# Optimization experiments

Hardware: AMD Instinct MI355X
Metric: run time of the kernel (lower is better)

Reference implementation:

```python
import jax, jax.numpy as jnp
import numpy as np

B, N, C = 64, 1024, 128


def setup_inputs() -> dict:
    key = jax.random.key(0)
    k1, k2, k3, k4, k5, k6 = jax.random.split(key, 6)
    adj_vals = jax.random.uniform(k1, (B, N, N), dtype=jnp.float32)
    mask = jax.random.uniform(k2, (B, N, N)) < 0.1
    adjacent = jnp.where(mask, adj_vals, 0.0)
    annotations = jax.random.normal(k3, (B, N, C), dtype=jnp.float32)
    # GraphConvolution bias, shape (1,1,C)
    gc_bias = jax.random.normal(k4, (1, 1, C), dtype=jnp.float32) * 0.05
    # Keras GRU params (reset_after=True default): kernel (C,3C), recurrent (C,3C), bias (2,3C)
    kernel = jax.random.normal(k5, (C, 3 * C), dtype=jnp.float32) / np.sqrt(C)
    recurrent_kernel = jax.random.normal(k6, (C, 3 * C), dtype=jnp.float32) / np.sqrt(C)
    gru_bias = jnp.zeros((2, 3 * C), dtype=jnp.float32)
    return {"adjacent": adjacent, "annotations": annotations, "gc_bias": gc_bias,
            "kernel": kernel, "recurrent_kernel": recurrent_kernel, "gru_bias": gru_bias}


def reference(adjacent, annotations, gc_bias, kernel, recurrent_kernel, gru_bias):
    # GraphConvolution: per-graph adj @ annotations, batched, + bias
    v = jnp.einsum('bij,bjc->bic', adjacent, annotations) + gc_bias  # [B,N,C]
    b, n, c = v.shape
    x = v.reshape(-1, c)            # visible states, one GRU step each
    h = annotations.reshape(-1, c)  # initial hidden states
    # single-step Keras GRU (reset_after=True)
    mx = x @ kernel + gru_bias[0]
    mh = h @ recurrent_kernel + gru_bias[1]
    xz, xr, xh = jnp.split(mx, 3, axis=-1)
    hz, hr, hh_in = jnp.split(mh, 3, axis=-1)
    z = jax.nn.sigmoid(xz + hz)
    r = jax.nn.sigmoid(xr + hr)
    hh = jnp.tanh(xh + r * hh_in)
    out = z * h + (1.0 - z) * hh
    return out.reshape(b, n, c)
```

## Files before the change

### kernel.cpp

```cpp
#include <hip/hip_runtime.h>

typedef unsigned short ushort_t;
typedef __attribute__((ext_vector_type(8))) short bf16x8;
typedef __attribute__((ext_vector_type(8))) unsigned short u16x8;
typedef __attribute__((ext_vector_type(4))) float f32x4;

#define B_ 64
#define N_ 1024
#define C_ 128

static __device__ __forceinline__ unsigned short f2bf(float f) {
  union { float f; unsigned int i; } v; v.f = f;
  unsigned int i = v.i;
  return (unsigned short)((i + 0x7FFFu + ((i >> 16) & 1u)) >> 16);
}
static __device__ __forceinline__ void split1(float x, ushort_t& h, ushort_t& l) {
  union { float f; unsigned int i; } u; u.f = x;
  h = (ushort_t)(u.i >> 16);
  union { unsigned int i; float f; } t; t.i = u.i & 0xFFFF0000u;
  union { float f; unsigned int i; } w; w.f = x - t.f;
  l = (ushort_t)(w.i >> 16);
}
static __device__ __forceinline__ bf16x8 as_bf(u16x8 v) {
  union { u16x8 u; bf16x8 b; } x; x.u = v; return x.b;
}
static __device__ __forceinline__ void gload_lds16(const void* g, void* l) {
  __builtin_amdgcn_global_load_lds((const __attribute__((address_space(1))) void*)g,
                                   (__attribute__((address_space(3))) void*)l,
                                   16, 0, 0);
}

#define PIPE_BAR(N) asm volatile("s_waitcnt vmcnt(" #N ")\n\ts_barrier" ::: "memory")
#define POST_BAR()  asm volatile("s_waitcnt lgkmcnt(0)\n\ts_barrier" ::: "memory")

__global__ __launch_bounds__(256) void tsplit(const float* __restrict__ src,
                                              ushort_t* __restrict__ dh,
                                              ushort_t* __restrict__ dl,
                                              int rows, int cols, long sb, long db) {
  __shared__ float tile[64][65];
  const int t = threadIdx.x;
  src += (long)blockIdx.z * sb;
  dh  += (long)blockIdx.z * db;
  dl  += (long)blockIdx.z * db;
  const int r0 = blockIdx.y * 64, c0 = blockIdx.x * 64;
#pragma unroll
  for (int p = 0; p < 4; ++p) {
    int row = p * 16 + (t >> 4), c4 = (t & 15) * 4;
    f32x4 v = *(const f32x4*)(src + (long)(r0 + row) * cols + c0 + c4);
#pragma unroll
    for (int j = 0; j < 4; ++j) tile[row][c4 + j] = v[j];
  }
  __syncthreads();
  const int oc = t >> 2;
#pragma unroll
  for (int p = 0; p < 2; ++p) {
    int ck = (t & 3) + p * 4;
    u16x8 vh, vl;
#pragma unroll
    for (int j = 0; j < 8; ++j) {
      ushort_t hj, lj;
      split1(tile[ck * 8 + j][oc], hj, lj);
      vh[j] = hj; vl[j] = lj;
    }
    long o = (long)(c0 + oc) * rows + r0 + ck * 8;
    *(u16x8*)(dh + o) = vh;
    *(u16x8*)(dl + o) = vl;
  }
}

__global__ __launch_bounds__(256, 2) void gc_gru(const float* __restrict__ adj,
                                                 const ushort_t* __restrict__ annTh,
                                                 const ushort_t* __restrict__ annTl,
                                                 const float* __restrict__ ann,
                                                 const float* __restrict__ gcb,
                                                 const ushort_t* __restrict__ kTh,
                                                 const ushort_t* __restrict__ kTl,
                                                 const ushort_t* __restrict__ rTh,
                                                 const float* __restrict__ gb,
                                                 float* __restrict__ out) {
  __shared__ __align__(16) float vlds[128 * 132];
  float* lds_all = vlds;

  const int tid = threadIdx.x;
  const int w = tid >> 6, lane = tid & 63;
  const int wr = w >> 1, wc = w & 1;
  const int swz = (blockIdx.x & 7) * 64 + (blockIdx.x >> 3);
  const int b = swz >> 3;
  const int m0 = (swz & 7) * 128;

  const float*    adjb = adj   + ((long)b * N_ + m0) * N_;
  const ushort_t* aThb = annTh + (long)b * C_ * N_;
  const ushort_t* aTlb = annTl + (long)b * C_ * N_;

  const int fr = lane & 15;
  const int kg = lane >> 4;

  const int aRow = lane >> 3;
  const int aCs  = (lane & 7) ^ aRow;
  const int bRow = lane >> 2;
  const int bCs  = (lane & 3) ^ ((lane >> 3) & 3);

  f32x4 acc[4][4] = {};

#define STAGE(Q, T)                                                            \
  {                                                                            \
    const int k0_ = (T) * 32;                                                  \
    float*    A_  = lds_all + (Q) * 8192;                                      \
    ushort_t* Bh_ = (ushort_t*)(lds_all + (Q) * 8192 + 4096);                  \
    ushort_t* Bl_ = (ushort_t*)(lds_all + (Q) * 8192 + 6144);                  \
    _Pragma("unroll")                                                          \
    for (int jj = 0; jj < 4; ++jj) {                                           \
      int j_ = w * 4 + jj;                                                     \
      gload_lds16(adjb + (long)(j_ * 8 + aRow) * N_ + k0_ + aCs * 4,           \
                  (void*)(A_ + j_ * 256));                                     \
    }                                                                          \
    _Pragma("unroll")                                                          \
    for (int jj = 0; jj < 2; ++jj) {                                           \
      int j_ = w * 2 + jj;                                                     \
      long so_ = (long)(j_ * 16 + bRow) * N_ + k0_ + bCs * 8;                  \
      gload_lds16(aThb + so_, (void*)(Bh_ + j_ * 512));                        \
      gload_lds16(aTlb + so_, (void*)(Bl_ + j_ * 512));                        \
    }                                                                          \
  }

#define COMPUTE(Q)                                                             \
  {                                                                            \
    const float*    A_  = lds_all + (Q) * 8192;                                \
    const ushort_t* Bh_ = (const ushort_t*)(lds_all + (Q) * 8192 + 4096);      \
    const ushort_t* Bl_ = (const ushort_t*)(lds_all + (Q) * 8192 + 6144);      \
    bf16x8 bh_[4], bl_[4], ah_[4], al_[4];                                     \
    _Pragma("unroll")                                                          \
    for (int ni = 0; ni < 4; ++ni) {                                           \
      int row_ = wc * 64 + ni * 16 + fr;                                       \
      int kb_ = (kg << 4) ^ ((((row_) >> 1) & 3) << 4);                        \
      bh_[ni] = *(const bf16x8*)((const char*)Bh_ + row_ * 64 + kb_);          \
      bl_[ni] = *(const bf16x8*)((const char*)Bl_ + row_ * 64 + kb_);          \
    }                                                                          \
    _Pragma("unroll")                                                          \
    for (int mi = 0; mi < 4; ++mi) {                                           \
      int row_ = wr * 64 + mi * 16 + fr;                                       \
      int b0_ = row_ * 128 + ((kg * 32) ^ ((row_ & 7) << 4));                  \
      f32x4 a0_ = *(const f32x4*)((const char*)A_ + b0_);                      \
      f32x4 a1_ = *(const f32x4*)((const char*)A_ + (b0_ ^ 16));               \
      u16x8 vh_, vl_;                                                          \
      _Pragma("unroll")                                                        \
      for (int j = 0; j < 4; ++j) {                                            \
        ushort_t hj_, lj_;                                                     \
        split1(a0_[j], hj_, lj_); vh_[j] = hj_;     vl_[j] = lj_;              \
        split1(a1_[j], hj_, lj_); vh_[4 + j] = hj_; vl_[4 + j] = lj_;          \
      }                                                                        \
      ah_[mi] = as_bf(vh_); al_[mi] = as_bf(vl_);                              \
    }                                                                          \
    _Pragma("unroll")                                                          \
    for (int mi = 0; mi < 4; ++mi)                                             \
      _Pragma("unroll")                                                        \
      for (int ni = 0; ni < 4; ++ni) {                                         \
        acc[mi][ni] = __builtin_amdgcn_mfma_f32_16x16x32_bf16(ah_[mi], bh_[ni], acc[mi][ni], 0, 0, 0); \
        acc[mi][ni] = __builtin_amdgcn_mfma_f32_16x16x32_bf16(al_[mi], bh_[ni], acc[mi][ni], 0, 0, 0); \
        acc[mi][ni] = __builtin_amdgcn_mfma_f32_16x16x32_bf16(ah_[mi], bl_[ni], acc[mi][ni], 0, 0, 0); \
      }                                                                        \
  }

  STAGE(0, 0)

#pragma unroll 1
  for (int t = 0; t < 31; ++t) {
    const int cur = t & 1;
    STAGE(cur ^ 1, t + 1)
    PIPE_BAR(8);
    COMPUTE(cur)
    POST_BAR();
  }
  PIPE_BAR(0);
  COMPUTE(1)
  __syncthreads();

#undef STAGE
#undef COMPUTE

#pragma unroll
  for (int ni = 0; ni < 4; ++ni) {
    int col = wc * 64 + ni * 16 + fr;
    float bias = gcb[col];
#pragma unroll
    for (int mi = 0; mi < 4; ++mi) {
      int row = wr * 64 + mi * 16 + kg * 4;
#pragma unroll
      for (int r = 0; r < 4; ++r)
        vlds[(row + r) * 132 + col] = acc[mi][ni][r] + bias;
    }
  }
  __syncthreads();

  const long grow = (long)b * N_ + m0 + w * 32;

  bf16x8 xh[2][4], xl[2][4], hh[2][4];
#pragma unroll
  for (int s = 0; s < 2; ++s)
#pragma unroll
    for (int kk = 0; kk < 4; ++kk) {
      int lo = (w * 32 + s * 16 + fr) * 132 + kk * 32 + kg * 8;
      f32x4 x0 = *(const f32x4*)&vlds[lo];
      f32x4 x1 = *(const f32x4*)&vlds[lo + 4];
      u16x8 th, tl;
#pragma unroll
      for (int j = 0; j < 4; ++j) {
        ushort_t hj, lj;
        split1(x0[j], hj, lj); th[j] = hj; tl[j] = lj;
        split1(x1[j], hj, lj); th[4 + j] = hj; tl[4 + j] = lj;
      }
      xh[s][kk] = as_bf(th); xl[s][kk] = as_bf(tl);
      const float* hrow = ann + (grow + s * 16 + fr) * C_ + kk * 32 + kg * 8;
      f32x4 h0 = *(const f32x4*)hrow;
      f32x4 h1 = *(const f32x4*)(hrow + 4);
      u16x8 hv;
#pragma unroll
      for (int j = 0; j < 4; ++j) { hv[j] = f2bf(h0[j]); hv[4 + j] = f2bf(h1[j]); }
      hh[s][kk] = as_bf(hv);
    }

#define GATE(G, AK0, AK1, AR0, AR1)                                                         \
  do {                                                                                      \
    const ushort_t* kh_ = kTh + (long)((G) * C_ + cb) * C_;                                 \
    const ushort_t* kl_ = kTl + (long)((G) * C_ + cb) * C_;                                 \
    const ushort_t* rh_ = rTh + (long)((G) * C_ + cb) * C_;                                 \
    bf16x8 KH[4], KL[4], RH[4];                                                             \
    _Pragma("unroll")                                                                       \
    for (int kk = 0; kk < 4; ++kk) {                                                        \
      int o_ = kk * 32 + kg * 8;                                                            \
      KH[kk] = *(const bf16x8*)(kh_ + o_);                                                  \
      KL[kk] = *(const bf16x8*)(kl_ + o_);                                                  \
      RH[kk] = *(const bf16x8*)(rh_ + o_);                                                  \
    }                                                                                       \
    _Pragma("unroll")                                                                       \
    for (int kk = 0; kk < 4; ++kk) {                                                        \
      AK0 = __builtin_amdgcn_mfma_f32_16x16x32_bf16(xh[0][kk], KH[kk], AK0, 0, 0, 0);       \
      AK1 = __builtin_amdgcn_mfma_f32_16x16x32_bf16(xh[1][kk], KH[kk], AK1, 0, 0, 0);       \
      AK0 = __builtin_amdgcn_mfma_f32_16x16x32_bf16(xl[0][kk], KH[kk], AK0, 0, 0, 0);       \
      AK1 = __builtin_amdgcn_mfma_f32_16x16x32_bf16(xl[1][kk], KH[kk], AK1, 0, 0, 0);       \
      AK0 = __builtin_amdgcn_mfma_f32_16x16x32_bf16(xh[0][kk], KL[kk], AK0, 0, 0, 0);       \
      AK1 = __builtin_amdgcn_mfma_f32_16x16x32_bf16(xh[1][kk], KL[kk], AK1, 0, 0, 0);       \
    }                                                                                       \
    _Pragma("unroll")                                                                       \
    for (int kk = 0; kk < 4; ++kk) {                                                        \
      AR0 = __builtin_amdgcn_mfma_f32_16x16x32_bf16(hh[0][kk], RH[kk], AR0, 0, 0, 0);       \
      AR1 = __builtin_amdgcn_mfma_f32_16x16x32_bf16(hh[1][kk], RH[kk], AR1, 0, 0, 0);       \
    }                                                                                       \
  } while (0)

#pragma unroll 1
  for (int n = 0; n < 8; ++n) {
    const int cb = n * 16 + fr;
    f32x4 az0 = {}, az1 = {}, ar0 = {}, ar1 = {}, ax0 = {}, ax1 = {}, ah0 = {}, ah1 = {};
    GATE(0, az0, az1, az0, az1);
    GATE(1, ar0, ar1, ar0, ar1);
    GATE(2, ax0, ax1, ah0, ah1);

    const float bz  = gb[cb] + gb[384 + cb];
    const float brr = gb[128 + cb] + gb[384 + 128 + cb];
    const float bxh = gb[256 + cb];
    const float bhi = gb[384 + 256 + cb];
#pragma unroll
    for (int s = 0; s < 2; ++s) {
      const f32x4& az_ = s ? az1 : az0;
      const f32x4& ar_ = s ? ar1 : ar0;
      const f32x4& ax_ = s ? ax1 : ax0;
      const f32x4& ah_ = s ? ah1 : ah0;
#pragma unroll
      for (int r = 0; r < 4; ++r) {
        long row = grow + s * 16 + kg * 4 + r;
        float hval = ann[row * C_ + cb];
        float zz = 1.f / (1.f + __expf(-(az_[r] + bz)));
        float rr = 1.f / (1.f + __expf(-(ar_[r] + brr)));
        float hpre = ax_[r] + bxh + rr * (ah_[r] + bhi);
        hpre = fminf(fmaxf(hpre, -15.f), 15.f);
        float e2 = __expf(2.f * hpre);
        float th = (e2 - 1.f) / (e2 + 1.f);
        out[row * C_ + cb] = zz * hval + (1.f - zz) * th;
      }
    }
  }
#undef GATE
}

extern "C" void kernel_launch(void* const* d_in, const int* in_sizes, int n_in,
                              void* d_out, int out_size, void* d_ws, size_t ws_size,
                              hipStream_t stream) {
  const float* adj = (const float*)d_in[0];
  const float* ann = (const float*)d_in[1];
  const float* gcb = (const float*)d_in[2];
  const float* ker = (const float*)d_in[3];
  const float* rk  = (const float*)d_in[4];
  const float* gb  = (const float*)d_in[5];
  float* out = (float*)d_out;

  char* ws = (char*)d_ws;
  ushort_t* annTh = (ushort_t*)(ws);
  ushort_t* annTl = (ushort_t*)(ws + 16777216);
  ushort_t* kTh   = (ushort_t*)(ws + 33554432);
  ushort_t* kTl   = (ushort_t*)(ws + 33652736);
  ushort_t* rTh   = (ushort_t*)(ws + 33751040);
  ushort_t* rTl   = (ushort_t*)(ws + 33849344);

  hipLaunchKernelGGL(tsplit, dim3(2, 16, 64), dim3(256), 0, stream,
                     ann, annTh, annTl, 1024, 128, (long)1024 * 128, (long)128 * 1024);
  hipLaunchKernelGGL(tsplit, dim3(6, 2, 1), dim3(256), 0, stream,
                     ker, kTh, kTl, 128, 384, 0L, 0L);
  hipLaunchKernelGGL(tsplit, dim3(6, 2, 1), dim3(256), 0, stream,
                     rk, rTh, rTl, 128, 384, 0L, 0L);
  hipLaunchKernelGGL(gc_gru, dim3(512), dim3(256), 0, stream,
                     adj, annTh, annTl, ann, gcb, kTh, kTl, rTh, gb, out);
}
```

Before: 163.8 us.

## Restructure GRU epilogue to keep gate weights in registers and pre-split x in LDS

The GRU epilogue is reorganised so each wave owns two 16-column output slices and holds all three gates' weight fragments in registers, looping over the 128 rows. The old layout reloaded the weights from global memory for every gate. The graph-convolution result is now split into bf16 hi/lo once and stored in a swizzled LDS layout, replacing the padded fp32 staging. The transpose kernel also writes a bf16 copy of the annotations so the hidden-state fragments no longer need conversion in the epilogue. Launch bounds drop to one block per SM, which frees registers for the weight fragments but may reduce occupancy for the main matmul loop.

```diff
diff --git a/kernel.cpp b/kernel.cpp
--- a/kernel.cpp
+++ b/kernel.cpp
@@ -3,6 +3,7 @@
 typedef unsigned short ushort_t;
 typedef __attribute__((ext_vector_type(8))) short bf16x8;
 typedef __attribute__((ext_vector_type(8))) unsigned short u16x8;
+typedef __attribute__((ext_vector_type(4))) unsigned short u16x4;
 typedef __attribute__((ext_vector_type(4))) float f32x4;
 
 #define B_ 64
@@ -36,7 +37,9 @@
 __global__ __launch_bounds__(256) void tsplit(const float* __restrict__ src,
                                               ushort_t* __restrict__ dh,
                                               ushort_t* __restrict__ dl,
-                                              int rows, int cols, long sb, long db) {
+                                              ushort_t* __restrict__ db2,
+                                              int rows, int cols, long sb, long db,
+                                              long db2s) {
   __shared__ float tile[64][65];
   const int t = threadIdx.x;
   src += (long)blockIdx.z * sb;
@@ -49,6 +52,12 @@
     f32x4 v = *(const f32x4*)(src + (long)(r0 + row) * cols + c0 + c4);
 #pragma unroll
     for (int j = 0; j < 4; ++j) tile[row][c4 + j] = v[j];
+    if (db2) {
+      u16x4 rb;
+#pragma unroll
+      for (int j = 0; j < 4; ++j) rb[j] = f2bf(v[j]);
+      *(u16x4*)(db2 + (long)blockIdx.z * db2s + (long)(r0 + row) * cols + c0 + c4) = rb;
+    }
   }
   __syncthreads();
   const int oc = t >> 2;
@@ -68,9 +77,10 @@
   }
 }
 
-__global__ __launch_bounds__(256, 2) void gc_gru(const float* __restrict__ adj,
+__global__ __launch_bounds__(256, 1) void gc_gru(const float* __restrict__ adj,
                                                  const ushort_t* __restrict__ annTh,
                                                  const ushort_t* __restrict__ annTl,
+                                                 const ushort_t* __restrict__ annB,
                                                  const float* __restrict__ ann,
                                                  const float* __restrict__ gcb,
                                                  const ushort_t* __restrict__ kTh,
@@ -78,8 +88,7 @@
                                                  const ushort_t* __restrict__ rTh,
                                                  const float* __restrict__ gb,
                                                  float* __restrict__ out) {
-  __shared__ __align__(16) float vlds[128 * 132];
-  float* lds_all = vlds;
+  __shared__ __align__(16) float lds_all[16384];
 
   const int tid = threadIdx.x;
   const int w = tid >> 6, lane = tid & 63;
@@ -94,7 +103,6 @@
 
   const int fr = lane & 15;
   const int kg = lane >> 4;
-
   const int aRow = lane >> 3;
   const int aCs  = (lane & 7) ^ aRow;
   const int bRow = lane >> 2;
@@ -162,7 +170,6 @@
   }
 
   STAGE(0, 0)
-
 #pragma unroll 1
   for (int t = 0; t < 31; ++t) {
     const int cur = t & 1;
@@ -178,101 +185,99 @@
 #undef STAGE
 #undef COMPUTE
 
+  ushort_t* ldsXh = (ushort_t*)lds_all;
+  ushort_t* ldsXl = ldsXh + 16384;
 #pragma unroll
   for (int ni = 0; ni < 4; ++ni) {
     int col = wc * 64 + ni * 16 + fr;
     float bias = gcb[col];
 #pragma unroll
     for (int mi = 0; mi < 4; ++mi) {
-      int row = wr * 64 + mi * 16 + kg * 4;
-#pragma unroll
-      for (int r = 0; r < 4; ++r)
-        vlds[(row + r) * 132 + col] = acc[mi][ni][r] + bias;
+#pragma unroll
+      for (int r = 0; r < 4; ++r) {
+        int row = wr * 64 + mi * 16 + kg * 4 + r;
+        ushort_t hq, lq;
+        split1(acc[mi][ni][r] + bias, hq, lq);
+        int off = row * 256 + ((((col >> 3) ^ (row & 7)) << 4)) + (col & 7) * 2;
+        *(ushort_t*)((char*)ldsXh + off) = hq;
+        *(ushort_t*)((char*)ldsXl + off) = lq;
+      }
     }
   }
   __syncthreads();
 
-  const long grow = (long)b * N_ + m0 + w * 32;
-
-  bf16x8 xh[2][4], xl[2][4], hh[2][4];
-#pragma unroll
-  for (int s = 0; s < 2; ++s)
-#pragma unroll
-    for (int kk = 0; kk < 4; ++kk) {
-      int lo = (w * 32 + s * 16 + fr) * 132 + kk * 32 + kg * 8;
-      f32x4 x0 = *(const f32x4*)&vlds[lo];
-      f32x4 x1 = *(const f32x4*)&vlds[lo + 4];
-      u16x8 th, tl;
-#pragma unroll
-      for (int j = 0; j < 4; ++j) {
-        ushort_t hj, lj;
-        split1(x0[j], hj, lj); th[j] = hj; tl[j] = lj;
-        split1(x1[j], hj, lj); th[4 + j] = hj; tl[4 + j] = lj;
-      }
-      xh[s][kk] = as_bf(th); xl[s][kk] = as_bf(tl);
-      const float* hrow = ann + (grow + s * 16 + fr) * C_ + kk * 32 + kg * 8;
-      f32x4 h0 = *(const f32x4*)hrow;
-      f32x4 h1 = *(const f32x4*)(hrow + 4);
-      u16x8 hv;
-#pragma unroll
-      for (int j = 0; j < 4; ++j) { hv[j] = f2bf(h0[j]); hv[4 + j] = f2bf(h1[j]); }
-      hh[s][kk] = as_bf(hv);
-    }
-
-#define GATE(G, AK0, AK1, AR0, AR1)                                                         \
-  do {                                                                                      \
-    const ushort_t* kh_ = kTh + (long)((G) * C_ + cb) * C_;                                 \
-    const ushort_t* kl_ = kTl + (long)((G) * C_ + cb) * C_;                                 \
-    const ushort_t* rh_ = rTh + (long)((G) * C_ + cb) * C_;                                 \
-    bf16x8 KH[4], KL[4], RH[4];                                                             \
-    _Pragma("unroll")                                                                       \
-    for (int kk = 0; kk < 4; ++kk) {                                                        \
-      int o_ = kk * 32 + kg * 8;                                                            \
-      KH[kk] = *(const bf16x8*)(kh_ + o_);                                                  \
-      KL[kk] = *(const bf16x8*)(kl_ + o_);                                                  \
-      RH[kk] = *(const bf16x8*)(rh_ + o_);                                                  \
-    }                                                                                       \
-    _Pragma("unroll")                                                                       \
-    for (int kk = 0; kk < 4; ++kk) {                                                        \
-      AK0 = __builtin_amdgcn_mfma_f32_16x16x32_bf16(xh[0][kk], KH[kk], AK0, 0, 0, 0);       \
-      AK1 = __builtin_amdgcn_mfma_f32_16x16x32_bf16(xh[1][kk], KH[kk], AK1, 0, 0, 0);       \
-      AK0 = __builtin_amdgcn_mfma_f32_16x16x32_bf16(xl[0][kk], KH[kk], AK0, 0, 0, 0);       \
-      AK1 = __builtin_amdgcn_mfma_f32_16x16x32_bf16(xl[1][kk], KH[kk], AK1, 0, 0, 0);       \
-      AK0 = __builtin_amdgcn_mfma_f32_16x16x32_bf16(xh[0][kk], KL[kk], AK0, 0, 0, 0);       \
-      AK1 = __builtin_amdgcn_mfma_f32_16x16x32_bf16(xh[1][kk], KL[kk], AK1, 0, 0, 0);       \
-    }                                                                                       \
-    _Pragma("unroll")                                                                       \
-    for (int kk = 0; kk < 4; ++kk) {                                                        \
-      AR0 = __builtin_amdgcn_mfma_f32_16x16x32_bf16(hh[0][kk], RH[kk], AR0, 0, 0, 0);       \
-      AR1 = __builtin_amdgcn_mfma_f32_16x16x32_bf16(hh[1][kk], RH[kk], AR1, 0, 0, 0);       \
-    }                                                                                       \
-  } while (0)
+  const long grow = (long)b * N_ + m0;
+  const int frk = fr & 7;
 
 #pragma unroll 1
-  for (int n = 0; n < 8; ++n) {
+  for (int nn = 0; nn < 2; ++nn) {
+    const int n = w * 2 + nn;
+    bf16x8 WKH[3][4], WKL[3][4], WRH[3][4];
+#pragma unroll
+    for (int g = 0; g < 3; ++g) {
+      const long wb = (long)(g * C_ + n * 16 + fr) * C_;
+#pragma unroll
+      for (int kk = 0; kk < 4; ++kk) {
+        int o_ = kk * 32 + kg * 8;
+        WKH[g][kk] = *(const bf16x8*)(kTh + wb + o_);
+        WKL[g][kk] = *(const bf16x8*)(kTl + wb + o_);
+        WRH[g][kk] = *(const bf16x8*)(rTh + wb + o_);
+      }
+    }
+
     const int cb = n * 16 + fr;
-    f32x4 az0 = {}, az1 = {}, ar0 = {}, ar1 = {}, ax0 = {}, ax1 = {}, ah0 = {}, ah1 = {};
-    GATE(0, az0, az1, az0, az1);
-    GATE(1, ar0, ar1, ar0, ar1);
-    GATE(2, ax0, ax1, ah0, ah1);
-
     const float bz  = gb[cb] + gb[384 + cb];
     const float brr = gb[128 + cb] + gb[384 + 128 + cb];
     const float bxh = gb[256 + cb];
     const float bhi = gb[384 + 256 + cb];
-#pragma unroll
-    for (int s = 0; s < 2; ++s) {
-      const f32x4& az_ = s ? az1 : az0;
-      const f32x4& ar_ = s ? ar1 : ar0;
-      const f32x4& ax_ = s ? ax1 : ax0;
-      const f32x4& ah_ = s ? ah1 : ah0;
+
+#pragma unroll 1
+    for (int s = 0; s < 8; ++s) {
+      const int lr = s * 16 + fr;
+      bf16x8 xhf[4], xlf[4], hhf[4];
+#pragma unroll
+      for (int kk = 0; kk < 4; ++kk) {
+        int off = lr * 256 + ((((kk * 4 + kg) ^ frk)) << 4);
+        xhf[kk] = *(const bf16x8*)((const char*)ldsXh + off);
+        xlf[kk] = *(const bf16x8*)((const char*)ldsXl + off);
+        hhf[kk] = *(const bf16x8*)(annB + (grow + lr) * (long)C_ + kk * 32 + kg * 8);
+      }
+      f32x4 az = {}, ar = {}, ax = {}, ah = {};
+#pragma unroll
+      for (int kk = 0; kk < 4; ++kk) {
+        az = __builtin_amdgcn_mfma_f32_16x16x32_bf16(xhf[kk], WKH[0][kk], az, 0, 0, 0);
+        az = __builtin_amdgcn_mfma_f32_16x16x32_bf16(xlf[kk], WKH[0][kk], az, 0, 0, 0);
+        az = __builtin_amdgcn_mfma_f32_16x16x32_bf16(xhf[kk], WKL[0][kk], az, 0, 0, 0);
+      }
+#pragma unroll
+      for (int kk = 0; kk < 4; ++kk)
+        az = __builtin_amdgcn_mfma_f32_16x16x32_bf16(hhf[kk], WRH[0][kk], az, 0, 0, 0);
+#pragma unroll
+      for (int kk = 0; kk < 4; ++kk) {
+        ar = __builtin_amdgcn_mfma_f32_16x16x32_bf16(xhf[kk], WKH[1][kk], ar, 0, 0, 0);
+        ar = __builtin_amdgcn_mfma_f32_16x16x32_bf16(xlf[kk], WKH[1][kk], ar, 0, 0, 0);
+        ar = __builtin_amdgcn_mfma_f32_16x16x32_bf16(xhf[kk], WKL[1][kk], ar, 0, 0, 0);
+      }
+#pragma unroll
+      for (int kk = 0; kk < 4; ++kk)
+        ar = __builtin_amdgcn_mfma_f32_16x16x32_bf16(hhf[kk], WRH[1][kk], ar, 0, 0, 0);
+#pragma unroll
+      for (int kk = 0; kk < 4; ++kk) {
+        ax = __builtin_amdgcn_mfma_f32_16x16x32_bf16(xhf[kk], WKH[2][kk], ax, 0, 0, 0);
+        ax = __builtin_amdgcn_mfma_f32_16x16x32_bf16(xlf[kk], WKH[2][kk], ax, 0, 0, 0);
+        ax = __builtin_amdgcn_mfma_f32_16x16x32_bf16(xhf[kk], WKL[2][kk], ax, 0, 0, 0);
+      }
+#pragma unroll
+      for (int kk = 0; kk < 4; ++kk)
+        ah = __builtin_amdgcn_mfma_f32_16x16x32_bf16(hhf[kk], WRH[2][kk], ah, 0, 0, 0);
+
 #pragma unroll
       for (int r = 0; r < 4; ++r) {
         long row = grow + s * 16 + kg * 4 + r;
-        float hval = ann[row * C_ + cb];
-        float zz = 1.f / (1.f + __expf(-(az_[r] + bz)));
-        float rr = 1.f / (1.f + __expf(-(ar_[r] + brr)));
-        float hpre = ax_[r] + bxh + rr * (ah_[r] + bhi);
+        float hval = ann[row * (long)C_ + cb];
+        float zz = 1.f / (1.f + __expf(-(az[r] + bz)));
+        float rr = 1.f / (1.f + __expf(-(ar[r] + brr)));
+        float hpre = ax[r] + bxh + rr * (ah[r] + bhi);
         hpre = fminf(fmaxf(hpre, -15.f), 15.f);
         float e2 = __expf(2.f * hpre);
         float th = (e2 - 1.f) / (e2 + 1.f);
@@ -280,7 +285,6 @@
       }
     }
   }
-#undef GATE
 }
 
 extern "C" void kernel_launch(void* const* d_in, const int* in_sizes, int n_in,
@@ -301,13 +305,15 @@
   ushort_t* kTl   = (ushort_t*)(ws + 33652736);
   ushort_t* rTh   = (ushort_t*)(ws + 33751040);
   ushort_t* rTl   = (ushort_t*)(ws + 33849344);
+  ushort_t* annB  = (ushort_t*)(ws + 33947648);
 
   hipLaunchKernelGGL(tsplit, dim3(2, 16, 64), dim3(256), 0, stream,
-                     ann, annTh, annTl, 1024, 128, (long)1024 * 128, (long)128 * 1024);
+                     ann, annTh, annTl, annB, 1024, 128,
+                     (long)1024 * 128, (long)128 * 1024, (long)1024 * 128);
   hipLaunchKernelGGL(tsplit, dim3(6, 2, 1), dim3(256), 0, stream,
-                     ker, kTh, kTl, 128, 384, 0L, 0L);
+                     ker, kTh, kTl, (ushort_t*)nullptr, 128, 384, 0L, 0L, 0L);
   hipLaunchKernelGGL(tsplit, dim3(6, 2, 1), dim3(256), 0, stream,
-                     rk, rTh, rTl, 128, 384, 0L, 0L);
+                     rk, rTh, rTl, (ushort_t*)nullptr, 128, 384, 0L, 0L, 0L);
   hipLaunchKernelGGL(gc_gru, dim3(512), dim3(256), 0, stream,
-                     adj, annTh, annTl, ann, gcb, kTh, kTl, rTh, gb, out);
-}
+                     adj, annTh, annTl, annB, ann, gcb, kTh, kTl, rTh, gb, out);
+}
```

After: 186.6 us. 13.9% more time.
